# Kernel tuning notes

Hardware: AMD Instinct MI355X
Metric: run time of the kernel (lower is better)

The kernel has to match this reference:

```python
import jax, jax.numpy as jnp
import numpy as np

T = 512        # sequence / max_length
I = 512        # input_dim
H = 1024       # hidden_size
O = 1          # output_size
L = 512        # max_length (attention logits)


def setup_inputs() -> dict:
    key = jax.random.key(0)
    ks = jax.random.split(key, 14)
    s = 0.02
    return {
        "input_seq": jax.random.normal(ks[0], (T, I), jnp.float32),
        "target_seq": jax.random.normal(ks[1], (T, O), jnp.float32),
        # encoder LSTM (input I -> hidden H), PyTorch gate order i,f,g,o
        "W_ih_e": jax.random.normal(ks[2], (4 * H, I), jnp.float32) * s,
        "W_hh_e": jax.random.normal(ks[3], (4 * H, H), jnp.float32) * s,
        "b_ih_e": jnp.zeros((4 * H,), jnp.float32),
        "b_hh_e": jnp.zeros((4 * H,), jnp.float32),
        # attention: Linear(2H -> L)
        "W_attn": jax.random.normal(ks[4], (L, 2 * H), jnp.float32) * s,
        "b_attn": jnp.zeros((L,), jnp.float32),
        # decoder LSTM (input 2H -> hidden H)
        "W_ih_d": jax.random.normal(ks[5], (4 * H, 2 * H), jnp.float32) * s,
        "W_hh_d": jax.random.normal(ks[6], (4 * H, H), jnp.float32) * s,
        "b_ih_d": jnp.zeros((4 * H,), jnp.float32),
        "b_hh_d": jnp.zeros((4 * H,), jnp.float32),
        # output Linear(H -> O)
        "W_out": jax.random.normal(ks[7], (O, H), jnp.float32) * s,
        "b_out": jnp.zeros((O,), jnp.float32),
    }


def _lstm_cell(x, h, c, Wih, Whh, bih, bhh):
    gates = Wih @ x + bih + Whh @ h + bhh          # [4H]
    i, f, g, o = jnp.split(gates, 4)
    c = jax.nn.sigmoid(f) * c + jax.nn.sigmoid(i) * jnp.tanh(g)
    h = jax.nn.sigmoid(o) * jnp.tanh(c)
    return h, c


def reference(input_seq, target_seq, W_ih_e, W_hh_e, b_ih_e, b_hh_e,
              W_attn, b_attn, W_ih_d, W_hh_d, b_ih_d, b_hh_d, W_out, b_out):
    Th = input_seq.shape[0]
    max_len = W_attn.shape[0]
    hid = W_hh_e.shape[1]

    def step(carry, xs):
        eh, ec, dh, dc, aw = carry
        x_t, i = xs
        eh, ec = _lstm_cell(x_t, eh, ec, W_ih_e, W_hh_e, b_ih_e, b_hh_e)
        energy = W_attn @ jnp.concatenate([eh, dh]) + b_attn   # [L]
        aw = aw.at[i].set(energy[i])
        aw = jax.nn.softmax(aw)                                 # re-softmaxed each step, as in source
        context = aw[i] * eh                                    # [H]
        din = jnp.concatenate([context, dh])                    # [2H]
        dh, dc = _lstm_cell(din, dh, dc, W_ih_d, W_hh_d, b_ih_d, b_hh_d)
        out_t = W_out @ dh + b_out                              # [O]
        return (eh, ec, dh, dc, aw), out_t

    z = jnp.zeros((hid,), input_seq.dtype)
    carry0 = (z, z, z, z, jnp.zeros((max_len,), input_seq.dtype))
    _, output_seq = jax.lax.scan(step, carry0, (input_seq, jnp.arange(Th)))
    return output_seq  # [T, O]
```

## Files before the change

### kernel.cpp

```cpp
#include <hip/hip_runtime.h>
#include <math.h>


#define T_STEPS 512
#define ENC_BLK 128
#define NBLK    256
#define NTHR    512
#define POLL_LIMIT 30000u

typedef float fv4 __attribute__((ext_vector_type(4)));

__device__ __forceinline__ float sigf(float x) { return 1.0f / (1.0f + expf(-x)); }

__device__ __forceinline__ float ld_f(const float* p) {
  return __hip_atomic_load(p, __ATOMIC_RELAXED, __HIP_MEMORY_SCOPE_AGENT);
}

__device__ __forceinline__ void st_bypass4(float* p, float v) {
  asm volatile("global_store_dword %0, %1, off sc0 sc1"
               :: "v"(p), "v"(v) : "memory");
}

__device__ __forceinline__ bool valid4(fv4 v) {
  return __float_as_uint(v.x) != 0xAAAAAAAAu && __float_as_uint(v.y) != 0xAAAAAAAAu &&
         __float_as_uint(v.z) != 0xAAAAAAAAu && __float_as_uint(v.w) != 0xAAAAAAAAu;
}
__device__ __forceinline__ bool validf(float a, float b, float c, float d) {
  return __float_as_uint(a) != 0xAAAAAAAAu && __float_as_uint(b) != 0xAAAAAAAAu &&
         __float_as_uint(c) != 0xAAAAAAAAu && __float_as_uint(d) != 0xAAAAAAAAu;
}

__device__ __forceinline__ fv4 poll2(const float* p, int* okp) {
  fv4 a, b;
  int ok = 1;
  asm volatile("global_load_dwordx4 %0, %1, off sc0 sc1" : "=v"(a) : "v"(p) : "memory");
  for (unsigned it = 0;; ++it) {
    asm volatile("global_load_dwordx4 %0, %1, off sc0 sc1" : "=v"(b) : "v"(p) : "memory");
    asm volatile("s_waitcnt vmcnt(1)" : "+v"(a) :: "memory");
    if (valid4(a)) { asm volatile("s_waitcnt vmcnt(0)" ::: "memory"); break; }
    asm volatile("global_load_dwordx4 %0, %1, off sc0 sc1" : "=v"(a) : "v"(p) : "memory");
    asm volatile("s_waitcnt vmcnt(1)" : "+v"(b) :: "memory");
    if (valid4(b)) { asm volatile("s_waitcnt vmcnt(0)" ::: "memory"); a = b; break; }
    if (it > POLL_LIMIT) { ok = 0; asm volatile("s_waitcnt vmcnt(0)" ::: "memory"); break; }
  }
  *okp = ok;
  return a;
}

__global__ __launch_bounds__(256) void prep_gemm(const float* __restrict__ X,
                                                 const float* __restrict__ Wih,
                                                 const float* __restrict__ bih,
                                                 const float* __restrict__ bhh,
                                                 float* __restrict__ px) {
  __shared__ float Ws[64][68];
  __shared__ float Xs[64][68];
  const int r0 = blockIdx.x * 64;
  const int t0 = blockIdx.y * 64;
  const int tid = threadIdx.x;
  const int tr = tid & 15;
  const int tc = tid >> 4;
  float acc[4][4] = {{0.f}};
  for (int k0 = 0; k0 < 512; k0 += 64) {
    __syncthreads();
    const int lr = tid >> 4;
    const int lc = (tid & 15) * 4;
#pragma unroll
    for (int rep = 0; rep < 4; rep++) {
      const int row = lr + rep * 16;
      const float4 wv = *(const float4*)&Wih[(size_t)(r0 + row) * 512 + k0 + lc];
      Ws[lc + 0][row] = wv.x; Ws[lc + 1][row] = wv.y;
      Ws[lc + 2][row] = wv.z; Ws[lc + 3][row] = wv.w;
      const float4 xv = *(const float4*)&X[(size_t)(t0 + row) * 512 + k0 + lc];
      Xs[row][lc + 0] = xv.x; Xs[row][lc + 1] = xv.y;
      Xs[row][lc + 2] = xv.z; Xs[row][lc + 3] = xv.w;
    }
    __syncthreads();
    for (int kk = 0; kk < 64; kk++) {
      float a[4], x[4];
#pragma unroll
      for (int i = 0; i < 4; i++) a[i] = Ws[kk][tr * 4 + i];
#pragma unroll
      for (int j = 0; j < 4; j++) x[j] = Xs[tc * 4 + j][kk];
#pragma unroll
      for (int i = 0; i < 4; i++)
#pragma unroll
        for (int j = 0; j < 4; j++) acc[i][j] += a[i] * x[j];
    }
  }
#pragma unroll
  for (int i = 0; i < 4; i++) {
    const int r = r0 + tr * 4 + i;
    const int g = r >> 10, h = r & 1023;
    const float bsum = bih[r] + bhh[r];
#pragma unroll
    for (int j = 0; j < 4; j++) {
      const int t = t0 + tc * 4 + j;
      px[((size_t)t * 1024 + h) * 4 + g] = acc[i][j] + bsum;
    }
  }
}

__global__ __launch_bounds__(512, 1) void lstm_persist(
    const float* __restrict__ Whhe, const float* __restrict__ Wattn,
    const float* __restrict__ battn, const float* __restrict__ Wihd,
    const float* __restrict__ Whhd, const float* __restrict__ bihd,
    const float* __restrict__ bhhd, const float* __restrict__ Wout,
    const float* __restrict__ bout, const float* __restrict__ px,
    float* ehbuf, float* dhbuf, float* out) {
  __shared__ float4 xbuf[256];
  __shared__ float4 dbuf[256];
  __shared__ float  aw[512];
  __shared__ float  GA[32];
  __shared__ float  GB[32];
  __shared__ float  bd[32];
  __shared__ float  redE[4];
  __shared__ float  redE2[4];
  __shared__ float  red[8];
  __shared__ float  red2[4];
  __shared__ int    sbad;

  const int b    = blockIdx.x;
  const int tid  = threadIdx.x;
  const int w    = tid >> 6;
  const int lane = tid & 63;
  const int ri   = lane & 3;
  const int s16  = lane >> 2;
  const int g    = w >> 1;
  const int j    = ((w & 1) << 2) + ri;

  if (b < ENC_BLK) {
    const int e = b;
    const int r = (g << 10) + (e << 3) + j;
    float4 we[16];
#pragma unroll
    for (int k = 0; k < 16; k++) {
      const int m = (k + s16) & 15;
      we[k] = *(const float4*)&Whhe[(size_t)r * 1024 + s16 * 64 + m * 4];
    }
    if (tid < 256) xbuf[tid] = make_float4(0.f, 0.f, 0.f, 0.f);
    if (tid == 0) sbad = 0;
    float ec = 0.f;
    __syncthreads();

    for (int t = 0; t < T_STEPS; t++) {
      float ge = 0.f;
#pragma unroll
      for (int k = 0; k < 16; k++) {
        const int m = (k + s16) & 15;
        const float4 x = xbuf[s16 * 16 + m];
        ge += we[k].x * x.x + we[k].y * x.y + we[k].z * x.z + we[k].w * x.w;
      }
      if (s16 == 0) ge += px[((size_t)t * 1024 + (e << 3) + j) * 4 + g];
      ge += __shfl_xor(ge, 4, 64);
      ge += __shfl_xor(ge, 8, 64);
      ge += __shfl_xor(ge, 16, 64);
      ge += __shfl_xor(ge, 32, 64);
      if (lane < 4) GA[w * 4 + lane] = ge;
      __syncthreads();
      if (tid < 8) {
        const float gi = GA[tid], gf = GA[8 + tid], gg = GA[16 + tid], go = GA[24 + tid];
        const float c = sigf(gf) * ec + sigf(gi) * tanhf(gg);
        ec = c;
        const float h = sigf(go) * tanhf(c);
        st_bypass4(&ehbuf[(size_t)t * 1024 + (e << 3) + tid], h);
      }
      int ok = 1;
      if (tid < 256) {
        const fv4 ev = poll2(&ehbuf[(size_t)t * 1024 + tid * 4], &ok);
        xbuf[tid] = make_float4(ev.x, ev.y, ev.z, ev.w);
      }
      if (!ok) sbad = 1;
      __syncthreads();
      if (sbad) break;
    }
  } else {
    const int d = b - ENC_BLK;
    const int r = (g << 10) + (d << 3) + j;
    float4 w1[16], wr[16];
#pragma unroll
    for (int k = 0; k < 16; k++) {
      const int m = (k + s16) & 15;
      w1[k] = *(const float4*)&Wihd[(size_t)r * 2048 + s16 * 64 + m * 4];
      const float4 a = *(const float4*)&Wihd[(size_t)r * 2048 + 1024 + s16 * 64 + m * 4];
      const float4 c = *(const float4*)&Whhd[(size_t)r * 1024 + s16 * 64 + m * 4];
      wr[k] = make_float4(a.x + c.x, a.y + c.y, a.z + c.z, a.w + c.w);
    }
    if (tid < 32) {
      const int gg2 = tid >> 3, jj2 = tid & 7;
      bd[tid] = bihd[(gg2 << 10) + (d << 3) + jj2] + bhhd[(gg2 << 10) + (d << 3) + jj2];
    }
    aw[tid] = 0.f;
    if (tid < 256) {
      xbuf[tid] = make_float4(0.f, 0.f, 0.f, 0.f);
      dbuf[tid] = make_float4(0.f, 0.f, 0.f, 0.f);
    }
    if (tid == 0) sbad = 0;
    float dc = 0.f;
    float4 wo = make_float4(0.f, 0.f, 0.f, 0.f);
    if (tid < 256) wo = *(const float4*)&Wout[tid * 4];
    const float boutv = bout[0];
    __syncthreads();

    float es0 = 0.f, es1 = 0.f, es2 = 0.f, es3 = 0.f;
    if (tid < 256) {
      const float* pe = &ehbuf[(size_t)tid * 4];
      es0 = ld_f(pe + 0); es1 = ld_f(pe + 1); es2 = ld_f(pe + 2); es3 = ld_f(pe + 3);
    }

    bool failed = false;
    for (int t = 0; t < T_STEPS; t++) {
      const float battn_t = battn[t];
      const float ex0 = expf(aw[tid]);
      float so = (tid == t) ? 0.f : ex0;
#pragma unroll
      for (int mk = 1; mk <= 32; mk <<= 1) so += __shfl_xor(so, mk, 64);
      if (lane == 0) red[w] = so;

      float4 wae = make_float4(0.f, 0.f, 0.f, 0.f);
      float4 wad = make_float4(0.f, 0.f, 0.f, 0.f);
      float epe = 0.f;
      int ok1 = 1;
      if (tid < 256) {
        wae = *(const float4*)&Wattn[(size_t)t * 2048 + tid * 4];
        wad = *(const float4*)&Wattn[(size_t)t * 2048 + 1024 + tid * 4];
        fv4 ev;
        if (validf(es0, es1, es2, es3)) {
          ev.x = es0; ev.y = es1; ev.z = es2; ev.w = es3;
        } else {
          ev = poll2(&ehbuf[(size_t)t * 1024 + tid * 4], &ok1);
        }
        epe = wae.x * ev.x + wae.y * ev.y + wae.z * ev.z + wae.w * ev.w;
        xbuf[tid] = make_float4(ev.x, ev.y, ev.z, ev.w);
      }
      if (!ok1) sbad = 1;
#pragma unroll
      for (int mk = 1; mk <= 32; mk <<= 1) epe += __shfl_xor(epe, mk, 64);
      if (lane == 0 && w < 4) redE[w] = epe;
      __syncthreads();
      if (sbad) { failed = true; break; }

      float ds0 = 0.f, ds1 = 0.f, ds2 = 0.f, ds3 = 0.f;
      if (t > 0 && tid < 256) {
        const float* pd = &dhbuf[(size_t)(t - 1) * 1024 + tid * 4];
        ds0 = ld_f(pd + 0); ds1 = ld_f(pd + 1); ds2 = ld_f(pd + 2); ds3 = ld_f(pd + 3);
      }

      float g1 = 0.f;
#pragma unroll
      for (int k = 0; k < 16; k++) {
        const int m = (k + s16) & 15;
        const float4 x = xbuf[s16 * 16 + m];
        g1 += w1[k].x * x.x + w1[k].y * x.y + w1[k].z * x.z + w1[k].w * x.w;
      }
      g1 += __shfl_xor(g1, 4, 64);
      g1 += __shfl_xor(g1, 8, 64);
      g1 += __shfl_xor(g1, 16, 64);
      g1 += __shfl_xor(g1, 32, 64);
      if (lane < 4) GA[w * 4 + lane] = g1;

      float epd = 0.f;
      int ok2 = 1;
      if (t > 0 && tid < 256) {
        fv4 dv;
        if (validf(ds0, ds1, ds2, ds3)) {
          dv.x = ds0; dv.y = ds1; dv.z = ds2; dv.w = ds3;
        } else {
          dv = poll2(&dhbuf[(size_t)(t - 1) * 1024 + tid * 4], &ok2);
        }
        epd = wad.x * dv.x + wad.y * dv.y + wad.z * dv.z + wad.w * dv.w;
        dbuf[tid] = make_float4(dv.x, dv.y, dv.z, dv.w);
      }
      if (!ok2) sbad = 1;
#pragma unroll
      for (int mk = 1; mk <= 32; mk <<= 1) epd += __shfl_xor(epd, mk, 64);
      if (lane == 0 && w < 4) redE2[w] = epd;
      __syncthreads();
      if (sbad) { failed = true; break; }

      float g2 = 0.f;
#pragma unroll
      for (int k = 0; k < 16; k++) {
        const int m = (k + s16) & 15;
        const float4 dd = dbuf[s16 * 16 + m];
        g2 += wr[k].x * dd.x + wr[k].y * dd.y + wr[k].z * dd.z + wr[k].w * dd.w;
      }
      g2 += __shfl_xor(g2, 4, 64);
      g2 += __shfl_xor(g2, 8, 64);
      g2 += __shfl_xor(g2, 16, 64);
      g2 += __shfl_xor(g2, 32, 64);
      if (lane < 4) GB[w * 4 + lane] = g2;

      const float e_t = redE[0] + redE[1] + redE[2] + redE[3] +
                        redE2[0] + redE2[1] + redE2[2] + redE2[3] + battn_t;
      const float exden = expf(e_t);
      const float inv = 1.f / (red[0] + red[1] + red[2] + red[3] +
                               red[4] + red[5] + red[6] + red[7] + exden);
      const float awt = exden * inv;
      aw[tid] = ((tid == t) ? exden : ex0) * inv;
      __syncthreads();

      if (tid < 8) {
        const float gi = awt * GA[tid]      + GB[tid]      + bd[tid];
        const float gf = awt * GA[8 + tid]  + GB[8 + tid]  + bd[8 + tid];
        const float gg = awt * GA[16 + tid] + GB[16 + tid] + bd[16 + tid];
        const float go = awt * GA[24 + tid] + GB[24 + tid] + bd[24 + tid];
        const float c = sigf(gf) * dc + sigf(gi) * tanhf(gg);
        dc = c;
        const float h = sigf(go) * tanhf(c);
        st_bypass4(&dhbuf[(size_t)t * 1024 + (d << 3) + tid], h);
      }

      if (tid < 256) {
        const int tn = (t + 1 < T_STEPS) ? (t + 1) : t;
        const float* pe = &ehbuf[(size_t)tn * 1024 + tid * 4];
        es0 = ld_f(pe + 0); es1 = ld_f(pe + 1); es2 = ld_f(pe + 2); es3 = ld_f(pe + 3);
      }
    }

    if (!failed) {
#pragma unroll
      for (int i = 0; i < 4; i++) {
        const int t = d * 4 + i;
        float op = 0.f;
        int ok = 1;
        if (tid < 256) {
          const fv4 dv = poll2(&dhbuf[(size_t)t * 1024 + tid * 4], &ok);
          op = wo.x * dv.x + wo.y * dv.y + wo.z * dv.z + wo.w * dv.w;
        }
        if (!ok) break;
#pragma unroll
        for (int mk = 1; mk <= 32; mk <<= 1) op += __shfl_xor(op, mk, 64);
        if (lane == 0 && w < 4) red2[w] = op;
        __syncthreads();
        if (tid == 0) out[t] = red2[0] + red2[1] + red2[2] + red2[3] + boutv;
        __syncthreads();
      }
    }
  }
}

extern "C" void kernel_launch(void* const* d_in, const int* in_sizes, int n_in,
                              void* d_out, int out_size, void* d_ws, size_t ws_size,
                              hipStream_t stream) {
  const float* X     = (const float*)d_in[0];
  const float* Wihe  = (const float*)d_in[2];
  const float* Whhe  = (const float*)d_in[3];
  const float* bihe  = (const float*)d_in[4];
  const float* bhhe  = (const float*)d_in[5];
  const float* Wattn = (const float*)d_in[6];
  const float* battn = (const float*)d_in[7];
  const float* Wihd  = (const float*)d_in[8];
  const float* Whhd  = (const float*)d_in[9];
  const float* bihd  = (const float*)d_in[10];
  const float* bhhd  = (const float*)d_in[11];
  const float* Wo    = (const float*)d_in[12];
  const float* bo    = (const float*)d_in[13];
  float* out = (float*)d_out;

  float* ws    = (float*)d_ws;
  float* px    = ws;
  float* ehbuf = px + (size_t)T_STEPS * 1024 * 4;
  float* dhbuf = ehbuf + (size_t)T_STEPS * 1024;
  const size_t need = ((size_t)T_STEPS * 1024 * 6) * sizeof(float);
  if (ws_size < need) return;

  prep_gemm<<<dim3(64, 8), 256, 0, stream>>>(X, Wihe, bihe, bhhe, px);
  lstm_persist<<<NBLK, NTHR, 0, stream>>>(
      Whhe, Wattn, battn, Wihd, Whhd, bihd, bhhd, Wo, bo, px, ehbuf, dhbuf, out);
}
```

Before: 1.824 ms.

## Split fused encoder/decoder persistent kernel into two sequential persistent kernels

The single persistent kernel ran 128 encoder blocks and 128 decoder blocks at the same time, with the decoder polling the encoder's hidden states step by step. The work now runs as two kernels: the encoder finishes all 512 steps first, then the decoder reads the finished encoder states with plain loads and no polling. This removes the cross-group polling and validity checks and shortens the decoder's per-step critical path. In exchange, encoder and decoder no longer overlap, so total time becomes the encoder time plus the decoder time.

```diff
diff --git a/kernel.cpp b/kernel.cpp
--- a/kernel.cpp
+++ b/kernel.cpp
@@ -3,9 +3,6 @@
 
 
 #define T_STEPS 512
-#define ENC_BLK 128
-#define NBLK    256
-#define NTHR    512
 #define POLL_LIMIT 30000u
 
 typedef float fv4 __attribute__((ext_vector_type(4)));
@@ -100,16 +97,77 @@
   }
 }
 
-__global__ __launch_bounds__(512, 1) void lstm_persist(
-    const float* __restrict__ Whhe, const float* __restrict__ Wattn,
-    const float* __restrict__ battn, const float* __restrict__ Wihd,
-    const float* __restrict__ Whhd, const float* __restrict__ bihd,
-    const float* __restrict__ bhhd, const float* __restrict__ Wout,
-    const float* __restrict__ bout, const float* __restrict__ px,
-    float* ehbuf, float* dhbuf, float* out) {
+__global__ __launch_bounds__(512, 1) void enc_persist(
+    const float* __restrict__ Whhe, const float* __restrict__ px,
+    float* ehbuf) {
+  __shared__ float4 xbuf[256];
+  __shared__ float  GA[32];
+  __shared__ int    sbad;
+
+  const int e    = blockIdx.x;
+  const int tid  = threadIdx.x;
+  const int w    = tid >> 6;
+  const int lane = tid & 63;
+  const int ri   = lane & 3;
+  const int s16  = lane >> 2;
+  const int g    = w >> 1;
+  const int j    = ((w & 1) << 2) + ri;
+
+  const int r = (g << 10) + (e << 3) + j;
+  float4 we[16];
+#pragma unroll
+  for (int k = 0; k < 16; k++) {
+    const int m = (k + s16) & 15;
+    we[k] = *(const float4*)&Whhe[(size_t)r * 1024 + s16 * 64 + m * 4];
+  }
+  if (tid < 256) xbuf[tid] = make_float4(0.f, 0.f, 0.f, 0.f);
+  if (tid == 0) sbad = 0;
+  float ec = 0.f;
+  __syncthreads();
+
+  for (int t = 0; t < T_STEPS; t++) {
+    float ge = 0.f;
+#pragma unroll
+    for (int k = 0; k < 16; k++) {
+      const int m = (k + s16) & 15;
+      const float4 x = xbuf[s16 * 16 + m];
+      ge += we[k].x * x.x + we[k].y * x.y + we[k].z * x.z + we[k].w * x.w;
+    }
+    if (s16 == 0) ge += px[((size_t)t * 1024 + (e << 3) + j) * 4 + g];
+    ge += __shfl_xor(ge, 4, 64);
+    ge += __shfl_xor(ge, 8, 64);
+    ge += __shfl_xor(ge, 16, 64);
+    ge += __shfl_xor(ge, 32, 64);
+    if (lane < 4) GA[w * 4 + lane] = ge;
+    __syncthreads();
+    if (tid < 8) {
+      const float gi = GA[tid], gf = GA[8 + tid], gg = GA[16 + tid], go = GA[24 + tid];
+      const float c = sigf(gf) * ec + sigf(gi) * tanhf(gg);
+      ec = c;
+      const float h = sigf(go) * tanhf(c);
+      st_bypass4(&ehbuf[(size_t)t * 1024 + (e << 3) + tid], h);
+    }
+    if (t + 1 < T_STEPS) {
+      int ok = 1;
+      if (tid < 256) {
+        const fv4 ev = poll2(&ehbuf[(size_t)t * 1024 + tid * 4], &ok);
+        xbuf[tid] = make_float4(ev.x, ev.y, ev.z, ev.w);
+      }
+      if (!ok) sbad = 1;
+      __syncthreads();
+      if (sbad) break;
+    }
+  }
+}
+
+__global__ __launch_bounds__(512, 1) void dec_persist(
+    const float* __restrict__ Wattn, const float* __restrict__ battn,
+    const float* __restrict__ Wihd, const float* __restrict__ Whhd,
+    const float* __restrict__ bihd, const float* __restrict__ bhhd,
+    const float* __restrict__ Wout, const float* __restrict__ bout,
+    const float* __restrict__ ehbuf, float* dhbuf, float* out) {
   __shared__ float4 xbuf[256];
   __shared__ float4 dbuf[256];
-  __shared__ float  aw[512];
   __shared__ float  GA[32];
   __shared__ float  GB[32];
   __shared__ float  bd[32];
@@ -119,7 +177,7 @@
   __shared__ float  red2[4];
   __shared__ int    sbad;
 
-  const int b    = blockIdx.x;
+  const int d    = blockIdx.x;
   const int tid  = threadIdx.x;
   const int w    = tid >> 6;
   const int lane = tid & 63;
@@ -128,213 +186,146 @@
   const int g    = w >> 1;
   const int j    = ((w & 1) << 2) + ri;
 
-  if (b < ENC_BLK) {
-    const int e = b;
-    const int r = (g << 10) + (e << 3) + j;
-    float4 we[16];
+  const int r = (g << 10) + (d << 3) + j;
+  float4 w1[16], wr[16];
+#pragma unroll
+  for (int k = 0; k < 16; k++) {
+    const int m = (k + s16) & 15;
+    w1[k] = *(const float4*)&Wihd[(size_t)r * 2048 + s16 * 64 + m * 4];
+    const float4 a = *(const float4*)&Wihd[(size_t)r * 2048 + 1024 + s16 * 64 + m * 4];
+    const float4 c = *(const float4*)&Whhd[(size_t)r * 1024 + s16 * 64 + m * 4];
+    wr[k] = make_float4(a.x + c.x, a.y + c.y, a.z + c.z, a.w + c.w);
+  }
+  if (tid < 32) {
+    const int gg2 = tid >> 3, jj2 = tid & 7;
+    bd[tid] = bihd[(gg2 << 10) + (d << 3) + jj2] + bhhd[(gg2 << 10) + (d << 3) + jj2];
+  }
+  float awreg = 0.f;
+  if (tid < 256) {
+    xbuf[tid] = make_float4(0.f, 0.f, 0.f, 0.f);
+    dbuf[tid] = make_float4(0.f, 0.f, 0.f, 0.f);
+  }
+  if (tid == 0) sbad = 0;
+  float dc = 0.f;
+  float4 wo = make_float4(0.f, 0.f, 0.f, 0.f);
+  if (tid < 256) wo = *(const float4*)&Wout[tid * 4];
+  const float boutv = bout[0];
+  __syncthreads();
+
+  bool failed = false;
+  for (int t = 0; t < T_STEPS; t++) {
+    float ds0 = 0.f, ds1 = 0.f, ds2 = 0.f, ds3 = 0.f;
+    if (t > 0 && tid < 256) {
+      const float* pd = &dhbuf[(size_t)(t - 1) * 1024 + tid * 4];
+      ds0 = ld_f(pd + 0); ds1 = ld_f(pd + 1); ds2 = ld_f(pd + 2); ds3 = ld_f(pd + 3);
+    }
+
+    float4 ev  = make_float4(0.f, 0.f, 0.f, 0.f);
+    float4 wae = make_float4(0.f, 0.f, 0.f, 0.f);
+    float4 wad = make_float4(0.f, 0.f, 0.f, 0.f);
+    if (tid < 256) {
+      ev  = *(const float4*)&ehbuf[(size_t)t * 1024 + tid * 4];
+      wae = *(const float4*)&Wattn[(size_t)t * 2048 + tid * 4];
+      wad = *(const float4*)&Wattn[(size_t)t * 2048 + 1024 + tid * 4];
+    }
+    const float battn_t = battn[t];
+
+    const float ex0 = expf(awreg);
+    float so = (tid == t) ? 0.f : ex0;
+#pragma unroll
+    for (int mk = 1; mk <= 32; mk <<= 1) so += __shfl_xor(so, mk, 64);
+    if (lane == 0) red[w] = so;
+
+    float epe = wae.x * ev.x + wae.y * ev.y + wae.z * ev.z + wae.w * ev.w;
+#pragma unroll
+    for (int mk = 1; mk <= 32; mk <<= 1) epe += __shfl_xor(epe, mk, 64);
+    if (lane == 0 && w < 4) redE[w] = epe;
+    if (tid < 256) xbuf[tid] = ev;
+    __syncthreads();
+
+    float g1 = 0.f;
 #pragma unroll
     for (int k = 0; k < 16; k++) {
       const int m = (k + s16) & 15;
-      we[k] = *(const float4*)&Whhe[(size_t)r * 1024 + s16 * 64 + m * 4];
-    }
-    if (tid < 256) xbuf[tid] = make_float4(0.f, 0.f, 0.f, 0.f);
-    if (tid == 0) sbad = 0;
-    float ec = 0.f;
-    __syncthreads();
-
-    for (int t = 0; t < T_STEPS; t++) {
-      float ge = 0.f;
-#pragma unroll
-      for (int k = 0; k < 16; k++) {
-        const int m = (k + s16) & 15;
-        const float4 x = xbuf[s16 * 16 + m];
-        ge += we[k].x * x.x + we[k].y * x.y + we[k].z * x.z + we[k].w * x.w;
+      const float4 x = xbuf[s16 * 16 + m];
+      g1 += w1[k].x * x.x + w1[k].y * x.y + w1[k].z * x.z + w1[k].w * x.w;
+    }
+    g1 += __shfl_xor(g1, 4, 64);
+    g1 += __shfl_xor(g1, 8, 64);
+    g1 += __shfl_xor(g1, 16, 64);
+    g1 += __shfl_xor(g1, 32, 64);
+    if (lane < 4) GA[w * 4 + lane] = g1;
+
+    float epd = 0.f;
+    int ok2 = 1;
+    if (t > 0 && tid < 256) {
+      fv4 dv;
+      if (validf(ds0, ds1, ds2, ds3)) {
+        dv.x = ds0; dv.y = ds1; dv.z = ds2; dv.w = ds3;
+      } else {
+        dv = poll2(&dhbuf[(size_t)(t - 1) * 1024 + tid * 4], &ok2);
       }
-      if (s16 == 0) ge += px[((size_t)t * 1024 + (e << 3) + j) * 4 + g];
-      ge += __shfl_xor(ge, 4, 64);
-      ge += __shfl_xor(ge, 8, 64);
-      ge += __shfl_xor(ge, 16, 64);
-      ge += __shfl_xor(ge, 32, 64);
-      if (lane < 4) GA[w * 4 + lane] = ge;
-      __syncthreads();
-      if (tid < 8) {
-        const float gi = GA[tid], gf = GA[8 + tid], gg = GA[16 + tid], go = GA[24 + tid];
-        const float c = sigf(gf) * ec + sigf(gi) * tanhf(gg);
-        ec = c;
-        const float h = sigf(go) * tanhf(c);
-        st_bypass4(&ehbuf[(size_t)t * 1024 + (e << 3) + tid], h);
-      }
+      epd = wad.x * dv.x + wad.y * dv.y + wad.z * dv.z + wad.w * dv.w;
+      dbuf[tid] = make_float4(dv.x, dv.y, dv.z, dv.w);
+    }
+    if (!ok2) sbad = 1;
+#pragma unroll
+    for (int mk = 1; mk <= 32; mk <<= 1) epd += __shfl_xor(epd, mk, 64);
+    if (lane == 0 && w < 4) redE2[w] = epd;
+    __syncthreads();
+    if (sbad) { failed = true; break; }
+
+    float g2 = 0.f;
+#pragma unroll
+    for (int k = 0; k < 16; k++) {
+      const int m = (k + s16) & 15;
+      const float4 dd = dbuf[s16 * 16 + m];
+      g2 += wr[k].x * dd.x + wr[k].y * dd.y + wr[k].z * dd.z + wr[k].w * dd.w;
+    }
+    g2 += __shfl_xor(g2, 4, 64);
+    g2 += __shfl_xor(g2, 8, 64);
+    g2 += __shfl_xor(g2, 16, 64);
+    g2 += __shfl_xor(g2, 32, 64);
+    if (lane < 4) GB[w * 4 + lane] = g2;
+
+    const float e_t = redE[0] + redE[1] + redE[2] + redE[3] +
+                      redE2[0] + redE2[1] + redE2[2] + redE2[3] + battn_t;
+    const float exden = expf(e_t);
+    const float inv = 1.f / (red[0] + red[1] + red[2] + red[3] +
+                             red[4] + red[5] + red[6] + red[7] + exden);
+    const float awt = exden * inv;
+    awreg = ((tid == t) ? exden : ex0) * inv;
+    __syncthreads();
+
+    if (tid < 8) {
+      const float gi = awt * GA[tid]      + GB[tid]      + bd[tid];
+      const float gf = awt * GA[8 + tid]  + GB[8 + tid]  + bd[8 + tid];
+      const float gg = awt * GA[16 + tid] + GB[16 + tid] + bd[16 + tid];
+      const float go = awt * GA[24 + tid] + GB[24 + tid] + bd[24 + tid];
+      const float c = sigf(gf) * dc + sigf(gi) * tanhf(gg);
+      dc = c;
+      const float h = sigf(go) * tanhf(c);
+      st_bypass4(&dhbuf[(size_t)t * 1024 + (d << 3) + tid], h);
+    }
+  }
+
+  if (!failed) {
+#pragma unroll
+    for (int i = 0; i < 4; i++) {
+      const int t = d * 4 + i;
+      float op = 0.f;
       int ok = 1;
       if (tid < 256) {
-        const fv4 ev = poll2(&ehbuf[(size_t)t * 1024 + tid * 4], &ok);
-        xbuf[tid] = make_float4(ev.x, ev.y, ev.z, ev.w);
+        const fv4 dv = poll2(&dhbuf[(size_t)t * 1024 + tid * 4], &ok);
+        op = wo.x * dv.x + wo.y * dv.y + wo.z * dv.z + wo.w * dv.w;
       }
-      if (!ok) sbad = 1;
+      if (!ok) break;
+#pragma unroll
+      for (int mk = 1; mk <= 32; mk <<= 1) op += __shfl_xor(op, mk, 64);
+      if (lane == 0 && w < 4) red2[w] = op;
       __syncthreads();
-      if (sbad) break;
-    }
-  } else {
-    const int d = b - ENC_BLK;
-    const int r = (g << 10) + (d << 3) + j;
-    float4 w1[16], wr[16];
-#pragma unroll
-    for (int k = 0; k < 16; k++) {
-      const int m = (k + s16) & 15;
-      w1[k] = *(const float4*)&Wihd[(size_t)r * 2048 + s16 * 64 + m * 4];
-      const float4 a = *(const float4*)&Wihd[(size_t)r * 2048 + 1024 + s16 * 64 + m * 4];
-      const float4 c = *(const float4*)&Whhd[(size_t)r * 1024 + s16 * 64 + m * 4];
-      wr[k] = make_float4(a.x + c.x, a.y + c.y, a.z + c.z, a.w + c.w);
-    }
-    if (tid < 32) {
-      const int gg2 = tid >> 3, jj2 = tid & 7;
-      bd[tid] = bihd[(gg2 << 10) + (d << 3) + jj2] + bhhd[(gg2 << 10) + (d << 3) + jj2];
-    }
-    aw[tid] = 0.f;
-    if (tid < 256) {
-      xbuf[tid] = make_float4(0.f, 0.f, 0.f, 0.f);
-      dbuf[tid] = make_float4(0.f, 0.f, 0.f, 0.f);
-    }
-    if (tid == 0) sbad = 0;
-    float dc = 0.f;
-    float4 wo = make_float4(0.f, 0.f, 0.f, 0.f);
-    if (tid < 256) wo = *(const float4*)&Wout[tid * 4];
-    const float boutv = bout[0];
-    __syncthreads();
-
-    float es0 = 0.f, es1 = 0.f, es2 = 0.f, es3 = 0.f;
-    if (tid < 256) {
-      const float* pe = &ehbuf[(size_t)tid * 4];
-      es0 = ld_f(pe + 0); es1 = ld_f(pe + 1); es2 = ld_f(pe + 2); es3 = ld_f(pe + 3);
-    }
-
-    bool failed = false;
-    for (int t = 0; t < T_STEPS; t++) {
-      const float battn_t = battn[t];
-      const float ex0 = expf(aw[tid]);
-      float so = (tid == t) ? 0.f : ex0;
-#pragma unroll
-      for (int mk = 1; mk <= 32; mk <<= 1) so += __shfl_xor(so, mk, 64);
-      if (lane == 0) red[w] = so;
-
-      float4 wae = make_float4(0.f, 0.f, 0.f, 0.f);
-      float4 wad = make_float4(0.f, 0.f, 0.f, 0.f);
-      float epe = 0.f;
-      int ok1 = 1;
-      if (tid < 256) {
-        wae = *(const float4*)&Wattn[(size_t)t * 2048 + tid * 4];
-        wad = *(const float4*)&Wattn[(size_t)t * 2048 + 1024 + tid * 4];
-        fv4 ev;
-        if (validf(es0, es1, es2, es3)) {
-          ev.x = es0; ev.y = es1; ev.z = es2; ev.w = es3;
-        } else {
-          ev = poll2(&ehbuf[(size_t)t * 1024 + tid * 4], &ok1);
-        }
-        epe = wae.x * ev.x + wae.y * ev.y + wae.z * ev.z + wae.w * ev.w;
-        xbuf[tid] = make_float4(ev.x, ev.y, ev.z, ev.w);
-      }
-      if (!ok1) sbad = 1;
-#pragma unroll
-      for (int mk = 1; mk <= 32; mk <<= 1) epe += __shfl_xor(epe, mk, 64);
-      if (lane == 0 && w < 4) redE[w] = epe;
+      if (tid == 0) out[t] = red2[0] + red2[1] + red2[2] + red2[3] + boutv;
       __syncthreads();
-      if (sbad) { failed = true; break; }
-
-      float ds0 = 0.f, ds1 = 0.f, ds2 = 0.f, ds3 = 0.f;
-      if (t > 0 && tid < 256) {
-        const float* pd = &dhbuf[(size_t)(t - 1) * 1024 + tid * 4];
-        ds0 = ld_f(pd + 0); ds1 = ld_f(pd + 1); ds2 = ld_f(pd + 2); ds3 = ld_f(pd + 3);
-      }
-
-      float g1 = 0.f;
-#pragma unroll
-      for (int k = 0; k < 16; k++) {
-        const int m = (k + s16) & 15;
-        const float4 x = xbuf[s16 * 16 + m];
-        g1 += w1[k].x * x.x + w1[k].y * x.y + w1[k].z * x.z + w1[k].w * x.w;
-      }
-      g1 += __shfl_xor(g1, 4, 64);
-      g1 += __shfl_xor(g1, 8, 64);
-      g1 += __shfl_xor(g1, 16, 64);
-      g1 += __shfl_xor(g1, 32, 64);
-      if (lane < 4) GA[w * 4 + lane] = g1;
-
-      float epd = 0.f;
-      int ok2 = 1;
-      if (t > 0 && tid < 256) {
-        fv4 dv;
-        if (validf(ds0, ds1, ds2, ds3)) {
-          dv.x = ds0; dv.y = ds1; dv.z = ds2; dv.w = ds3;
-        } else {
-          dv = poll2(&dhbuf[(size_t)(t - 1) * 1024 + tid * 4], &ok2);
-        }
-        epd = wad.x * dv.x + wad.y * dv.y + wad.z * dv.z + wad.w * dv.w;
-        dbuf[tid] = make_float4(dv.x, dv.y, dv.z, dv.w);
-      }
-      if (!ok2) sbad = 1;
-#pragma unroll
-      for (int mk = 1; mk <= 32; mk <<= 1) epd += __shfl_xor(epd, mk, 64);
-      if (lane == 0 && w < 4) redE2[w] = epd;
-      __syncthreads();
-      if (sbad) { failed = true; break; }
-
-      float g2 = 0.f;
-#pragma unroll
-      for (int k = 0; k < 16; k++) {
-        const int m = (k + s16) & 15;
-        const float4 dd = dbuf[s16 * 16 + m];
-        g2 += wr[k].x * dd.x + wr[k].y * dd.y + wr[k].z * dd.z + wr[k].w * dd.w;
-      }
-      g2 += __shfl_xor(g2, 4, 64);
-      g2 += __shfl_xor(g2, 8, 64);
-      g2 += __shfl_xor(g2, 16, 64);
-      g2 += __shfl_xor(g2, 32, 64);
-      if (lane < 4) GB[w * 4 + lane] = g2;
-
-      const float e_t = redE[0] + redE[1] + redE[2] + redE[3] +
-                        redE2[0] + redE2[1] + redE2[2] + redE2[3] + battn_t;
-      const float exden = expf(e_t);
-      const float inv = 1.f / (red[0] + red[1] + red[2] + red[3] +
-                               red[4] + red[5] + red[6] + red[7] + exden);
-      const float awt = exden * inv;
-      aw[tid] = ((tid == t) ? exden : ex0) * inv;
-      __syncthreads();
-
-      if (tid < 8) {
-        const float gi = awt * GA[tid]      + GB[tid]      + bd[tid];
-        const float gf = awt * GA[8 + tid]  + GB[8 + tid]  + bd[8 + tid];
-        const float gg = awt * GA[16 + tid] + GB[16 + tid] + bd[16 + tid];
-        const float go = awt * GA[24 + tid] + GB[24 + tid] + bd[24 + tid];
-        const float c = sigf(gf) * dc + sigf(gi) * tanhf(gg);
-        dc = c;
-        const float h = sigf(go) * tanhf(c);
-        st_bypass4(&dhbuf[(size_t)t * 1024 + (d << 3) + tid], h);
-      }
-
-      if (tid < 256) {
-        const int tn = (t + 1 < T_STEPS) ? (t + 1) : t;
-        const float* pe = &ehbuf[(size_t)tn * 1024 + tid * 4];
-        es0 = ld_f(pe + 0); es1 = ld_f(pe + 1); es2 = ld_f(pe + 2); es3 = ld_f(pe + 3);
-      }
-    }
-
-    if (!failed) {
-#pragma unroll
-      for (int i = 0; i < 4; i++) {
-        const int t = d * 4 + i;
-        float op = 0.f;
-        int ok = 1;
-        if (tid < 256) {
-          const fv4 dv = poll2(&dhbuf[(size_t)t * 1024 + tid * 4], &ok);
-          op = wo.x * dv.x + wo.y * dv.y + wo.z * dv.z + wo.w * dv.w;
-        }
-        if (!ok) break;
-#pragma unroll
-        for (int mk = 1; mk <= 32; mk <<= 1) op += __shfl_xor(op, mk, 64);
-        if (lane == 0 && w < 4) red2[w] = op;
-        __syncthreads();
-        if (tid == 0) out[t] = red2[0] + red2[1] + red2[2] + red2[3] + boutv;
-        __syncthreads();
-      }
     }
   }
 }
@@ -365,6 +356,7 @@
   if (ws_size < need) return;
 
   prep_gemm<<<dim3(64, 8), 256, 0, stream>>>(X, Wihe, bihe, bhhe, px);
-  lstm_persist<<<NBLK, NTHR, 0, stream>>>(
-      Whhe, Wattn, battn, Wihd, Whhd, bihd, bhhd, Wo, bo, px, ehbuf, dhbuf, out);
-}
+  enc_persist<<<128, 512, 0, stream>>>(Whhe, px, ehbuf);
+  dec_persist<<<128, 512, 0, stream>>>(Wattn, battn, Wihd, Whhd, bihd, bhhd,
+                                       Wo, bo, ehbuf, dhbuf, out);
+}
```

New measurement: 3.223 ms. 76.7% more time.

## Add adaptive timed back-off before polling cross-block hidden-state flags

Applied to the files above, without the earlier changes.

Replaces immediate spin-polling of the encoder and decoder hidden-state buffers with an adaptive wait. Each block measures its step period with s_memrealtime, sleeps until a predicted ready time, then does a single load. It falls back to polling on a miss and adjusts the wait window based on whether every thread hit. The aim is to cut memory-system contention from many blocks polling at once, at the risk of adding idle latency on the serial recurrence critical path when the prediction is too long.

```diff
diff --git a/kernel.cpp b/kernel.cpp
--- a/kernel.cpp
+++ b/kernel.cpp
@@ -7,8 +7,10 @@
 #define NBLK    256
 #define NTHR    512
 #define POLL_LIMIT 30000u
+#define SPIN_LIMIT 200000
 
 typedef float fv4 __attribute__((ext_vector_type(4)));
+typedef unsigned long long u64;
 
 __device__ __forceinline__ float sigf(float x) { return 1.0f / (1.0f + expf(-x)); }
 
@@ -45,6 +47,19 @@
   }
   *okp = ok;
   return a;
+}
+
+__device__ __forceinline__ fv4 ld_once4(const float* p) {
+  fv4 a;
+  asm volatile("global_load_dwordx4 %0, %1, off sc0 sc1" : "=v"(a) : "v"(p) : "memory");
+  asm volatile("s_waitcnt vmcnt(0)" : "+v"(a) :: "memory");
+  return a;
+}
+
+__device__ __forceinline__ void spin_until(u64 tgt) {
+  int g = 0;
+  while (__builtin_amdgcn_s_memrealtime() < tgt && ++g < SPIN_LIMIT)
+    __builtin_amdgcn_s_sleep(1);
 }
 
 __global__ __launch_bounds__(256) void prep_gemm(const float* __restrict__ X,
@@ -140,6 +155,7 @@
     if (tid < 256) xbuf[tid] = make_float4(0.f, 0.f, 0.f, 0.f);
     if (tid == 0) sbad = 0;
     float ec = 0.f;
+    u64 rp_prev = 0, P = 0, W = 0;
     __syncthreads();
 
     for (int t = 0; t < T_STEPS; t++) {
@@ -164,13 +180,27 @@
         const float h = sigf(go) * tanhf(c);
         st_bypass4(&ehbuf[(size_t)t * 1024 + (e << 3) + tid], h);
       }
-      int ok = 1;
+      const u64 rp = __builtin_amdgcn_s_memrealtime();
+      if (t >= 1) {
+        u64 pm = rp - rp_prev;
+        if (t == 1) P = pm;
+        else { if (pm > (P << 1)) pm = P << 1; P = P - (P >> 2) + (pm >> 2); }
+        if (t == 2) W = (P >> 2) + (P >> 4);
+      }
+      rp_prev = rp;
+      int ok = 1, myhit = 1;
       if (tid < 256) {
-        const fv4 ev = poll2(&ehbuf[(size_t)t * 1024 + tid * 4], &ok);
+        if (W) spin_until(rp + W);
+        fv4 ev = ld_once4(&ehbuf[(size_t)t * 1024 + tid * 4]);
+        if (!valid4(ev)) { myhit = 0; ev = poll2(&ehbuf[(size_t)t * 1024 + tid * 4], &ok); }
         xbuf[tid] = make_float4(ev.x, ev.y, ev.z, ev.w);
       }
       if (!ok) sbad = 1;
-      __syncthreads();
+      const int allhit = __syncthreads_and(myhit);
+      if (t >= 2) {
+        if (allhit) { const u64 dn = P >> 6; W -= (W < dn ? W : dn); }
+        else        { W += (P >> 5); if (W > P) W = P; }
+      }
       if (sbad) break;
     }
   } else {
@@ -196,6 +226,7 @@
     }
     if (tid == 0) sbad = 0;
     float dc = 0.f;
+    u64 rpd_prev = 0, Pd = 0, Wd = 0;
     float4 wo = make_float4(0.f, 0.f, 0.f, 0.f);
     if (tid < 256) wo = *(const float4*)&Wout[tid * 4];
     const float boutv = bout[0];
@@ -239,11 +270,14 @@
       __syncthreads();
       if (sbad) { failed = true; break; }
 
-      float ds0 = 0.f, ds1 = 0.f, ds2 = 0.f, ds3 = 0.f;
-      if (t > 0 && tid < 256) {
-        const float* pd = &dhbuf[(size_t)(t - 1) * 1024 + tid * 4];
-        ds0 = ld_f(pd + 0); ds1 = ld_f(pd + 1); ds2 = ld_f(pd + 2); ds3 = ld_f(pd + 3);
-      }
+      const u64 rpd = __builtin_amdgcn_s_memrealtime();
+      if (t >= 1) {
+        u64 pm = rpd - rpd_prev;
+        if (t == 1) Pd = pm;
+        else { if (pm > (Pd << 1)) pm = Pd << 1; Pd = Pd - (Pd >> 2) + (pm >> 2); }
+        if (t == 2) Wd = (Pd >> 2);
+      }
+      rpd_prev = rpd;
 
       float g1 = 0.f;
 #pragma unroll
@@ -259,14 +293,11 @@
       if (lane < 4) GA[w * 4 + lane] = g1;
 
       float epd = 0.f;
-      int ok2 = 1;
+      int ok2 = 1, myhit2 = 1;
       if (t > 0 && tid < 256) {
-        fv4 dv;
-        if (validf(ds0, ds1, ds2, ds3)) {
-          dv.x = ds0; dv.y = ds1; dv.z = ds2; dv.w = ds3;
-        } else {
-          dv = poll2(&dhbuf[(size_t)(t - 1) * 1024 + tid * 4], &ok2);
-        }
+        if (Wd) spin_until(rpd + Wd);
+        fv4 dv = ld_once4(&dhbuf[(size_t)(t - 1) * 1024 + tid * 4]);
+        if (!valid4(dv)) { myhit2 = 0; dv = poll2(&dhbuf[(size_t)(t - 1) * 1024 + tid * 4], &ok2); }
         epd = wad.x * dv.x + wad.y * dv.y + wad.z * dv.z + wad.w * dv.w;
         dbuf[tid] = make_float4(dv.x, dv.y, dv.z, dv.w);
       }
@@ -274,7 +305,11 @@
 #pragma unroll
       for (int mk = 1; mk <= 32; mk <<= 1) epd += __shfl_xor(epd, mk, 64);
       if (lane == 0 && w < 4) redE2[w] = epd;
-      __syncthreads();
+      const int allhit2 = __syncthreads_and(myhit2);
+      if (t >= 3) {
+        if (allhit2) { const u64 dn = Pd >> 6; Wd -= (Wd < dn ? Wd : dn); }
+        else         { Wd += (Pd >> 5); if (Wd > Pd) Wd = Pd; }
+      }
       if (sbad) { failed = true; break; }
 
       float g2 = 0.f;
```

Measured after the change: 2.069 ms. 13.4% more time.
